# Performance work log

Measured on AMD Instinct MI355X. Metric: run time of the kernel, lower is better.

The kernel has to match this reference:

```python
import jax, jax.numpy as jnp
import numpy as np

Q = 127.0  # int8 absmax quantization denominator


def _make_quant_weight(key, out_dim, in_dim):
    """Emulate bitsandbytes Linear8bitLt weight: int8 matrix + per-row absmax scale."""
    k1, k2 = jax.random.split(key)
    w_fp = jax.random.normal(k1, (out_dim, in_dim), dtype=jnp.float32) * 0.02
    scale = jnp.max(jnp.abs(w_fp), axis=1)  # [out_dim] per-row absmax
    w_int8 = jnp.clip(jnp.round(w_fp / scale[:, None] * Q), -127, 127).astype(jnp.int8)
    return w_int8, scale


def setup_inputs() -> dict:
    key = jax.random.key(0)
    ks = jax.random.split(key, 4)
    B, S, H, I = 4, 1024, 5120, 12288
    x = jax.random.normal(ks[0], (B, S, H), dtype=jnp.float32)
    w_gate, s_gate = _make_quant_weight(ks[1], I, H)
    w_up, s_up = _make_quant_weight(ks[2], I, H)
    w_down, s_down = _make_quant_weight(ks[3], H, I)
    return {"x": x, "w_gate": w_gate, "s_gate": s_gate,
            "w_up": w_up, "s_up": s_up,
            "w_down": w_down, "s_down": s_down}


def _qlinear(x, w_int8, scale):
    # y = x @ dequant(W)^T ; dequant(W) = w_int8 * scale/127 per output row.
    # Fold scale after the matmul (equivalent, avoids materializing dequant W twice).
    y = jnp.einsum("bsh,oh->bso", x, w_int8.astype(x.dtype))
    return y * (scale / Q)


def reference(x, w_gate, s_gate, w_up, s_up, w_down, s_down):
    gate = jax.nn.silu(_qlinear(x, w_gate, s_gate))  # [B,S,I]
    up = _qlinear(x, w_up, s_up)                     # [B,S,I]
    return _qlinear(gate * up, w_down, s_down)       # [B,S,H]
```

## Files before the change

kernel.cpp:

```cpp
#include <hip/hip_runtime.h>
#include <hip/hip_bf16.h>
#include <stdint.h>

typedef unsigned short u16;
typedef __attribute__((ext_vector_type(4))) float floatx4;
typedef __attribute__((ext_vector_type(8))) short bf16x8;
typedef const __attribute__((address_space(1))) void gvoid;
typedef __attribute__((address_space(3))) void lvoid;

static constexpr int Mdim = 4096;
static constexpr int Hdim = 5120;
static constexpr int Idim = 12288;
static constexpr float QINV = 1.0f / 127.0f;

__global__ void conv_i32_to_bf16(const int* __restrict__ in, u16* __restrict__ out) {
    int idx = (blockIdx.x * 256 + threadIdx.x) * 4;
    int4 v = *(const int4*)(in + idx);
    __hip_bfloat16 b0 = __float2bfloat16((float)v.x);
    __hip_bfloat16 b1 = __float2bfloat16((float)v.y);
    __hip_bfloat16 b2 = __float2bfloat16((float)v.z);
    __hip_bfloat16 b3 = __float2bfloat16((float)v.w);
    ushort4 o;
    o.x = *(u16*)&b0; o.y = *(u16*)&b1; o.z = *(u16*)&b2; o.w = *(u16*)&b3;
    *(ushort4*)(out + idx) = o;
}

__global__ void conv_f32_to_bf16(const float* __restrict__ in, u16* __restrict__ out) {
    int idx = (blockIdx.x * 256 + threadIdx.x) * 4;
    float4 v = *(const float4*)(in + idx);
    __hip_bfloat16 b0 = __float2bfloat16(v.x);
    __hip_bfloat16 b1 = __float2bfloat16(v.y);
    __hip_bfloat16 b2 = __float2bfloat16(v.z);
    __hip_bfloat16 b3 = __float2bfloat16(v.w);
    ushort4 o;
    o.x = *(u16*)&b0; o.y = *(u16*)&b1; o.z = *(u16*)&b2; o.w = *(u16*)&b3;
    *(ushort4*)(out + idx) = o;
}

template<int MODE>
__global__ __launch_bounds__(256)
void gemm_bt(const u16* __restrict__ A, const u16* __restrict__ Bw,
             const float* __restrict__ scale, u16* __restrict__ GateBuf,
             float* __restrict__ OutF, int N, int K)
{
    constexpr int BM = 128, BN = 128, BK = 64;
    __shared__ u16 As[BM * BK];
    __shared__ u16 Bs[BN * BK];
    const int tid  = threadIdx.x;
    const int lane = tid & 63;
    const int wave = tid >> 6;
    const int row0 = blockIdx.x * BM;
    const int col0 = blockIdx.y * BN;
    const int wm = (wave & 1) * 64;
    const int wn = (wave >> 1) * 64;
    const int lm = lane & 15;
    const int lg = lane >> 4;

    floatx4 acc[4][4];
    #pragma unroll
    for (int i = 0; i < 4; i++)
        #pragma unroll
        for (int j = 0; j < 4; j++)
            acc[i][j] = (floatx4){0.f, 0.f, 0.f, 0.f};

    const u16* Ablk = A  + (size_t)row0 * K;
    const u16* Bblk = Bw + (size_t)col0 * K;

    for (int kt = 0; kt < K; kt += BK) {
        __syncthreads();
        #pragma unroll
        for (int i = 0; i < 4; i++) {
            int slot = i * 256 + tid;
            int r = slot >> 3;
            int u = slot & 7;
            int c = (u ^ (r & 7)) * 8;
            __builtin_amdgcn_global_load_lds((gvoid*)(Ablk + (size_t)r * K + kt + c),
                                             (lvoid*)(As + slot * 8), 16, 0, 0);
            __builtin_amdgcn_global_load_lds((gvoid*)(Bblk + (size_t)r * K + kt + c),
                                             (lvoid*)(Bs + slot * 8), 16, 0, 0);
        }
        __syncthreads();
        #pragma unroll
        for (int kk = 0; kk < BK; kk += 32) {
            bf16x8 af[4], bfr[4];
            #pragma unroll
            for (int i = 0; i < 4; i++) {
                const int rA = wm + i * 16 + lm;
                const int rB = wn + i * 16 + lm;
                const int uu = ((kk >> 3) + lg);
                af[i]  = *(const bf16x8*)(As + rA * BK + ((uu ^ (lm & 7)) << 3));
                bfr[i] = *(const bf16x8*)(Bs + rB * BK + ((uu ^ (lm & 7)) << 3));
            }
            #pragma unroll
            for (int i = 0; i < 4; i++)
                #pragma unroll
                for (int j = 0; j < 4; j++)
                    acc[i][j] = __builtin_amdgcn_mfma_f32_16x16x32_bf16(af[i], bfr[j], acc[i][j], 0, 0, 0);
        }
    }

    const int ln = lane & 15;
    const int rq = (lane >> 4) * 4;
    #pragma unroll
    for (int j = 0; j < 4; j++) {
        const int col = col0 + wn + j * 16 + ln;
        const float s = scale[col] * QINV;
        #pragma unroll
        for (int i = 0; i < 4; i++) {
            const int rowb = row0 + wm + i * 16 + rq;
            #pragma unroll
            for (int r = 0; r < 4; r++) {
                const size_t idx = (size_t)(rowb + r) * N + col;
                float v = acc[i][j][r] * s;
                if (MODE == 0) {
                    float g = v / (1.0f + __expf(-v));
                    __hip_bfloat16 h = __float2bfloat16(g);
                    GateBuf[idx] = *(u16*)&h;
                } else if (MODE == 1) {
                    u16 gu = GateBuf[idx];
                    float g = __bfloat162float(*(__hip_bfloat16*)&gu);
                    __hip_bfloat16 h = __float2bfloat16(g * v);
                    GateBuf[idx] = *(u16*)&h;
                } else {
                    OutF[idx] = v;
                }
            }
        }
    }
}

extern "C" void kernel_launch(void* const* d_in, const int* in_sizes, int n_in,
                              void* d_out, int out_size, void* d_ws, size_t ws_size,
                              hipStream_t stream)
{
    const float* x  = (const float*)d_in[0];
    const int*   wg = (const int*)d_in[1];
    const float* sg = (const float*)d_in[2];
    const int*   wu = (const int*)d_in[3];
    const float* su = (const float*)d_in[4];
    const int*   wd = (const int*)d_in[5];
    const float* sd = (const float*)d_in[6];
    float* out = (float*)d_out;

    char* ws = (char*)d_ws;
    u16* xb   = (u16*)ws;
    u16* wb   = (u16*)(ws + 41943040);
    u16* gate = (u16*)(ws + 41943040 + 125829120);

    conv_f32_to_bf16<<<20480, 256, 0, stream>>>(x, xb);

    conv_i32_to_bf16<<<61440, 256, 0, stream>>>(wg, wb);
    gemm_bt<0><<<dim3(Mdim / 128, Idim / 128), 256, 0, stream>>>(xb, wb, sg, gate, nullptr, Idim, Hdim);

    conv_i32_to_bf16<<<61440, 256, 0, stream>>>(wu, wb);
    gemm_bt<1><<<dim3(Mdim / 128, Idim / 128), 256, 0, stream>>>(xb, wb, su, gate, nullptr, Idim, Hdim);

    conv_i32_to_bf16<<<61440, 256, 0, stream>>>(wd, wb);
    gemm_bt<2><<<dim3(Mdim / 128, Hdim / 128), 256, 0, stream>>>(gate, wb, sd, nullptr, out, Hdim, Idim);
}
```

Baseline: 2.926 ms.

## Fuse gate and up projections into one GEMM with SiLU-multiply epilogue

Adds a gemm_gateup kernel that loads each activation tile once and multiplies it against both the gate and up weight tiles, keeping two accumulator sets. The epilogue applies SiLU to the gate result, multiplies by the up result and writes the bf16 product directly. This removes the second pass over the activations and the write-then-read round trip of the intermediate gate buffer. Both weight matrices are converted to bf16 up front, so the workspace must hold two converted weight buffers. The old three-GEMM path is kept as a fallback when the workspace is too small. The fused kernel doubles accumulator registers and uses more LDS per block, which can lower occupancy.

```diff
diff --git a/kernel.cpp b/kernel.cpp
--- a/kernel.cpp
+++ b/kernel.cpp
@@ -35,6 +35,111 @@
     ushort4 o;
     o.x = *(u16*)&b0; o.y = *(u16*)&b1; o.z = *(u16*)&b2; o.w = *(u16*)&b3;
     *(ushort4*)(out + idx) = o;
+}
+
+__global__ __launch_bounds__(256)
+void gemm_gateup(const u16* __restrict__ A, const u16* __restrict__ Bg,
+                 const u16* __restrict__ Bu, const float* __restrict__ sg,
+                 const float* __restrict__ su, u16* __restrict__ H,
+                 int N, int K)
+{
+    constexpr int BM = 128, BN = 128, BK = 64;
+    __shared__ u16 As[BM * BK];
+    __shared__ u16 Bgs[BN * BK];
+    __shared__ u16 Bus[BN * BK];
+    const int tid  = threadIdx.x;
+    const int lane = tid & 63;
+    const int wave = tid >> 6;
+    const int row0 = blockIdx.x * BM;
+    const int col0 = blockIdx.y * BN;
+    const int wm = (wave & 1) * 64;
+    const int wn = (wave >> 1) * 64;
+    const int lm = lane & 15;
+    const int lg = lane >> 4;
+
+    floatx4 accg[4][4], accu[4][4];
+    #pragma unroll
+    for (int i = 0; i < 4; i++)
+        #pragma unroll
+        for (int j = 0; j < 4; j++) {
+            accg[i][j] = (floatx4){0.f, 0.f, 0.f, 0.f};
+            accu[i][j] = (floatx4){0.f, 0.f, 0.f, 0.f};
+        }
+
+    const u16* Ablk  = A  + (size_t)row0 * K;
+    const u16* Bgblk = Bg + (size_t)col0 * K;
+    const u16* Bublk = Bu + (size_t)col0 * K;
+
+    for (int kt = 0; kt < K; kt += BK) {
+        __syncthreads();
+        #pragma unroll
+        for (int i = 0; i < 4; i++) {
+            int slot = i * 256 + tid;
+            int r = slot >> 3;
+            int u = slot & 7;
+            int c = (u ^ (r & 7)) * 8;
+            __builtin_amdgcn_global_load_lds((gvoid*)(Ablk + (size_t)r * K + kt + c),
+                                             (lvoid*)(As + slot * 8), 16, 0, 0);
+            __builtin_amdgcn_global_load_lds((gvoid*)(Bgblk + (size_t)r * K + kt + c),
+                                             (lvoid*)(Bgs + slot * 8), 16, 0, 0);
+            __builtin_amdgcn_global_load_lds((gvoid*)(Bublk + (size_t)r * K + kt + c),
+                                             (lvoid*)(Bus + slot * 8), 16, 0, 0);
+        }
+        __syncthreads();
+        #pragma unroll
+        for (int kk = 0; kk < BK; kk += 32) {
+            const int uu = (kk >> 3) + lg;
+            const int xo = ((uu ^ (lm & 7)) << 3);
+            bf16x8 af[4];
+            #pragma unroll
+            for (int i = 0; i < 4; i++)
+                af[i] = *(const bf16x8*)(As + (wm + i * 16 + lm) * BK + xo);
+            {
+                bf16x8 bf[4];
+                #pragma unroll
+                for (int j = 0; j < 4; j++)
+                    bf[j] = *(const bf16x8*)(Bgs + (wn + j * 16 + lm) * BK + xo);
+                #pragma unroll
+                for (int i = 0; i < 4; i++)
+                    #pragma unroll
+                    for (int j = 0; j < 4; j++)
+                        accg[i][j] = __builtin_amdgcn_mfma_f32_16x16x32_bf16(af[i], bf[j], accg[i][j], 0, 0, 0);
+            }
+            {
+                bf16x8 bf[4];
+                #pragma unroll
+                for (int j = 0; j < 4; j++)
+                    bf[j] = *(const bf16x8*)(Bus + (wn + j * 16 + lm) * BK + xo);
+                #pragma unroll
+                for (int i = 0; i < 4; i++)
+                    #pragma unroll
+                    for (int j = 0; j < 4; j++)
+                        accu[i][j] = __builtin_amdgcn_mfma_f32_16x16x32_bf16(af[i], bf[j], accu[i][j], 0, 0, 0);
+            }
+        }
+    }
+
+    const int ln = lane & 15;
+    const int rq = (lane >> 4) * 4;
+    #pragma unroll
+    for (int j = 0; j < 4; j++) {
+        const int col = col0 + wn + j * 16 + ln;
+        const float sgv = sg[col] * QINV;
+        const float suv = su[col] * QINV;
+        #pragma unroll
+        for (int i = 0; i < 4; i++) {
+            const int rowb = row0 + wm + i * 16 + rq;
+            #pragma unroll
+            for (int r = 0; r < 4; r++) {
+                const size_t idx = (size_t)(rowb + r) * N + col;
+                float g = accg[i][j][r] * sgv;
+                float u = accu[i][j][r] * suv;
+                float h = (g / (1.0f + __expf(-g))) * u;
+                __hip_bfloat16 hb = __float2bfloat16(h);
+                H[idx] = *(u16*)&hb;
+            }
+        }
+    }
 }
 
 template<int MODE>
@@ -82,14 +187,13 @@
         __syncthreads();
         #pragma unroll
         for (int kk = 0; kk < BK; kk += 32) {
+            const int uu = (kk >> 3) + lg;
+            const int xo = ((uu ^ (lm & 7)) << 3);
             bf16x8 af[4], bfr[4];
             #pragma unroll
             for (int i = 0; i < 4; i++) {
-                const int rA = wm + i * 16 + lm;
-                const int rB = wn + i * 16 + lm;
-                const int uu = ((kk >> 3) + lg);
-                af[i]  = *(const bf16x8*)(As + rA * BK + ((uu ^ (lm & 7)) << 3));
-                bfr[i] = *(const bf16x8*)(Bs + rB * BK + ((uu ^ (lm & 7)) << 3));
+                af[i]  = *(const bf16x8*)(As + (wm + i * 16 + lm) * BK + xo);
+                bfr[i] = *(const bf16x8*)(Bs + (wn + i * 16 + lm) * BK + xo);
             }
             #pragma unroll
             for (int i = 0; i < 4; i++)
@@ -143,18 +247,40 @@
     float* out = (float*)d_out;
 
     char* ws = (char*)d_ws;
-    u16* xb   = (u16*)ws;
-    u16* wb   = (u16*)(ws + 41943040);
-    u16* gate = (u16*)(ws + 41943040 + 125829120);
-
+    const size_t XB_BYTES = 41943040;
+    const size_t WB_BYTES = 125829120;
+    const size_t H_BYTES  = 100663296;
+
+    u16* xb = (u16*)ws;
     conv_f32_to_bf16<<<20480, 256, 0, stream>>>(x, xb);
 
-    conv_i32_to_bf16<<<61440, 256, 0, stream>>>(wg, wb);
-    gemm_bt<0><<<dim3(Mdim / 128, Idim / 128), 256, 0, stream>>>(xb, wb, sg, gate, nullptr, Idim, Hdim);
-
-    conv_i32_to_bf16<<<61440, 256, 0, stream>>>(wu, wb);
-    gemm_bt<1><<<dim3(Mdim / 128, Idim / 128), 256, 0, stream>>>(xb, wb, su, gate, nullptr, Idim, Hdim);
-
-    conv_i32_to_bf16<<<61440, 256, 0, stream>>>(wd, wb);
-    gemm_bt<2><<<dim3(Mdim / 128, Hdim / 128), 256, 0, stream>>>(gate, wb, sd, nullptr, out, Hdim, Idim);
-}
+    if (ws_size >= XB_BYTES + 2 * WB_BYTES + H_BYTES) {
+        u16* wbg = (u16*)(ws + XB_BYTES);
+        u16* wbu = (u16*)(ws + XB_BYTES + WB_BYTES);
+        u16* h   = (u16*)(ws + XB_BYTES + 2 * WB_BYTES);
+
+        conv_i32_to_bf16<<<61440, 256, 0, stream>>>(wg, wbg);
+        conv_i32_to_bf16<<<61440, 256, 0, stream>>>(wu, wbu);
+        gemm_gateup<<<dim3(Mdim / 128, Idim / 128), 256, 0, stream>>>(
+            xb, wbg, wbu, sg, su, h, Idim, Hdim);
+
+        conv_i32_to_bf16<<<61440, 256, 0, stream>>>(wd, wbg);
+        gemm_bt<2><<<dim3(Mdim / 128, Hdim / 128), 256, 0, stream>>>(
+            h, wbg, sd, nullptr, out, Hdim, Idim);
+    } else {
+        u16* wb   = (u16*)(ws + XB_BYTES);
+        u16* gate = (u16*)(ws + XB_BYTES + WB_BYTES);
+
+        conv_i32_to_bf16<<<61440, 256, 0, stream>>>(wg, wb);
+        gemm_bt<0><<<dim3(Mdim / 128, Idim / 128), 256, 0, stream>>>(
+            xb, wb, sg, gate, nullptr, Idim, Hdim);
+
+        conv_i32_to_bf16<<<61440, 256, 0, stream>>>(wu, wb);
+        gemm_bt<1><<<dim3(Mdim / 128, Idim / 128), 256, 0, stream>>>(
+            xb, wb, su, gate, nullptr, Idim, Hdim);
+
+        conv_i32_to_bf16<<<61440, 256, 0, stream>>>(wd, wb);
+        gemm_bt<2><<<dim3(Mdim / 128, Hdim / 128), 256, 0, stream>>>(
+            gate, wb, sd, nullptr, out, Hdim, Idim);
+    }
+}
```

Result: slower. 3.526 ms (+20.5%).
